# Kernel tuning notes

Measured on AMD Instinct MI355X. Metric: run time of the kernel, lower is better.

The kernel has to match this reference:

```python
import jax, jax.numpy as jnp
import numpy as np

B, S, HID = 2, 2048, 2048
NH, NKV, D = 32, 8, 128
EPS = 1e-06
ROPE_BASE = 1000000.0


def _rope_tables(seq_len, dim, base):
    inv_freq = 1.0 / (base ** (jnp.arange(0, dim, 2, dtype=jnp.float32) / dim))
    t = jnp.arange(seq_len, dtype=jnp.float32)
    freqs = jnp.einsum('i,j->ij', t, inv_freq)          # [S, D/2]
    emb = jnp.concatenate([freqs, freqs], axis=-1)      # [S, D]
    return emb[None, None].astype(jnp.float32)          # [1,1,S,D] (pre cos/sin)


def setup_inputs() -> dict:
    key = jax.random.key(0)
    ks = jax.random.split(key, 6)
    emb = _rope_tables(S, D, ROPE_BASE)
    return {
        'hidden_states': jax.random.normal(ks[0], (B, S, HID), jnp.float32),
        'cos': jnp.cos(emb),
        'sin': jnp.sin(emb),
        'wq': jax.random.normal(ks[1], (NH * D, HID), jnp.float32) * 0.02,
        'wk': jax.random.normal(ks[2], (NKV * D, HID), jnp.float32) * 0.02,
        'wv': jax.random.normal(ks[3], (NKV * D, HID), jnp.float32) * 0.02,
        'wo': jax.random.normal(ks[4], (HID, NH * D), jnp.float32) * 0.02,
        'q_norm_w': jnp.ones((D,), jnp.float32),
        'k_norm_w': jnp.ones((D,), jnp.float32),
    }


def _rmsnorm(x, w, eps=EPS):
    xf = x.astype(jnp.float32)
    var = jnp.mean(xf * xf, axis=-1, keepdims=True)
    return (w * (xf * jax.lax.rsqrt(var + eps))).astype(x.dtype)


def _rotate_half(x):
    x1, x2 = jnp.split(x, 2, axis=-1)
    return jnp.concatenate([-x2, x1], axis=-1)


def reference(hidden_states, cos, sin, wq, wk, wv, wo, q_norm_w, k_norm_w):
    b, s, _ = hidden_states.shape
    groups = NH // NKV
    # projections -> [b, heads, s, d]
    q = (hidden_states @ wq.T).reshape(b, s, NH, D).transpose(0, 2, 1, 3)
    k = (hidden_states @ wk.T).reshape(b, s, NKV, D).transpose(0, 2, 1, 3)
    v = (hidden_states @ wv.T).reshape(b, s, NKV, D).transpose(0, 2, 1, 3)
    # per-head RMSNorm then RoPE
    q = _rmsnorm(q, q_norm_w)
    k = _rmsnorm(k, k_norm_w)
    q = q * cos + _rotate_half(q) * sin
    k = k * cos + _rotate_half(k) * sin
    # GQA expansion (repeat_interleave on head dim)
    k = jnp.repeat(k, groups, axis=1)
    v = jnp.repeat(v, groups, axis=1)
    # attention scores with additive causal bias of -10000 (as in source)
    scores = jnp.einsum('bhqd,bhkd->bhqk', q, k) / jnp.sqrt(jnp.float32(D))
    mask = jnp.triu(jnp.ones((s, s), jnp.float32), k=1)
    scores = scores - mask * 10000.0
    attn = jax.nn.softmax(scores.astype(jnp.float32), axis=-1).astype(q.dtype)
    out = jnp.einsum('bhqk,bhkd->bhqd', attn, v)
    out = out.transpose(0, 2, 1, 3).reshape(b, s, NH * D)
    return out @ wo.T
```

## Files before the change

kernel.cpp:

```cpp
#include <hip/hip_runtime.h>

typedef unsigned short u16;
typedef __attribute__((ext_vector_type(8))) short bf16x8;
typedef __attribute__((ext_vector_type(4))) float f32x4;
typedef __attribute__((ext_vector_type(2))) unsigned int u32x2;
typedef __attribute__((ext_vector_type(4))) unsigned int u32x4;

#define GAS __attribute__((address_space(1)))
#define LAS __attribute__((address_space(3)))
#define MFMA __builtin_amdgcn_mfma_f32_16x16x32_bf16
#define BAR() __builtin_amdgcn_s_barrier()
#define WAITV(n) asm volatile("s_waitcnt vmcnt(" #n ")" ::: "memory")

__device__ __forceinline__ void gload16(const void* g, void* l) {
  __builtin_amdgcn_global_load_lds((GAS void*)g, (LAS void*)l, 16, 0, 0);
}
__device__ __forceinline__ u16 f2b(float x) {
  union { float f; unsigned u; } c; c.f = x;
  unsigned r = c.u + 0x7fffu + ((c.u >> 16) & 1u);
  return (u16)(r >> 16);
}
__device__ __forceinline__ float b2f(u16 h) {
  union { unsigned u; float f; } c; c.u = ((unsigned)h) << 16;
  return c.f;
}
__device__ __forceinline__ unsigned cvtpk(float lo, float hi) {
  unsigned r;
  asm("v_cvt_pk_bf16_f32 %0, %1, %2" : "=v"(r) : "v"(lo), "v"(hi));
  return r;
}

__global__ __launch_bounds__(256) void cvt_bf16(const float* __restrict__ src,
                                                u16* __restrict__ dst, int n8) {
  int i = blockIdx.x * 256 + threadIdx.x;
  if (i >= n8) return;
  const float4* s4 = (const float4*)src;
  float4 a = s4[(size_t)i * 2], b = s4[(size_t)i * 2 + 1];
  u32x4 v;
  v[0] = (unsigned)f2b(a.x) | ((unsigned)f2b(a.y) << 16);
  v[1] = (unsigned)f2b(a.z) | ((unsigned)f2b(a.w) << 16);
  v[2] = (unsigned)f2b(b.x) | ((unsigned)f2b(b.y) << 16);
  v[3] = (unsigned)f2b(b.z) | ((unsigned)f2b(b.w) << 16);
  *(u32x4*)(dst + (size_t)i * 8) = v;
}

template <int MODE>
__global__ __launch_bounds__(512, 2) void gemm256(
    const u16* __restrict__ A, const u16* __restrict__ B,
    u16* __restrict__ Dq, u16* __restrict__ Dk, u16* __restrict__ Dv,
    float* __restrict__ Dout, int K, int tilesN, int nwg) {
  __shared__ __attribute__((aligned(16))) u16 lds[2][2][2][128 * 64];
  const int tid = threadIdx.x;
  const int lane = tid & 63;
  const int w = tid >> 6;
  const int wr = w >> 2, wc = w & 3;
  const int r = lane & 15, g = lane >> 4;

  int wg = blockIdx.x;
  const int cpx = nwg >> 3;
  wg = (wg & 7) * cpx + (wg >> 3);
  const int bx = wg % tilesN, by = wg / tilesN;
  const size_t m0 = (size_t)by * 256, n0 = (size_t)bx * 256;
  const int NT = K >> 6;

  auto stage = [&](int dbuf, int op, int half, int c, int k0) {
    int slot = c * 512 + tid;
    int row = slot >> 3;
    int kg = (slot & 7) ^ (row & 7);
    const u16* src = (op == 0)
        ? A + (m0 + half * 128 + row) * (size_t)K + k0 + kg * 8
        : B + (n0 + half * 128 + row) * (size_t)K + k0 + kg * 8;
    gload16(src, (char*)&lds[dbuf][op][half][0] + c * 8192 + w * 1024);
  };
  auto ldA = [&](int cur, int mi, int kk) -> bf16x8 {
    int rowl = mi * 16 + r;
    return *(const bf16x8*)((const char*)&lds[cur][0][wr][0] + rowl * 128 +
                            (((kk << 2) + g) ^ (rowl & 7)) * 16);
  };
  auto ldB = [&](int cur, int ni, int kk) -> bf16x8 {
    int rowl = (wc & 1) * 64 + ni * 16 + r;
    return *(const bf16x8*)((const char*)&lds[cur][1][wc >> 1][0] + rowl * 128 +
                            (((kk << 2) + g) ^ (rowl & 7)) * 16);
  };

  f32x4 acc[8][4];
#pragma unroll
  for (int i = 0; i < 8; ++i)
#pragma unroll
    for (int j = 0; j < 4; ++j) acc[i][j] = (f32x4){0.f, 0.f, 0.f, 0.f};

  stage(0, 1, 0, 0, 0); stage(0, 1, 0, 1, 0);
  stage(0, 1, 1, 0, 0); stage(0, 1, 1, 1, 0);
  stage(0, 0, 0, 0, 0); stage(0, 0, 1, 0, 0);
  stage(0, 0, 0, 1, 0); stage(0, 0, 1, 1, 0);
  WAITV(2);
  BAR();

  bf16x8 bf_[4][2];

#define GPHASE(MI0, IS0, IS1, WAITCODE)                                    \
  {                                                                        \
    bf16x8 aA0 = ldA(cur, MI0, 0), aA1 = ldA(cur, MI0, 1);                 \
    bf16x8 aB0 = ldA(cur, MI0 + 1, 0), aB1 = ldA(cur, MI0 + 1, 1);         \
    IS0; IS1;                                                              \
    BAR();                                                                 \
    __builtin_amdgcn_s_setprio(1);                                         \
    _Pragma("unroll") for (int ni = 0; ni < 4; ++ni) {                     \
      acc[MI0][ni] = MFMA(aA0, bf_[ni][0], acc[MI0][ni], 0, 0, 0);         \
      acc[MI0][ni] = MFMA(aA1, bf_[ni][1], acc[MI0][ni], 0, 0, 0);         \
      acc[MI0 + 1][ni] = MFMA(aB0, bf_[ni][0], acc[MI0 + 1][ni], 0, 0, 0); \
      acc[MI0 + 1][ni] = MFMA(aB1, bf_[ni][1], acc[MI0 + 1][ni], 0, 0, 0); \
    }                                                                      \
    __builtin_amdgcn_s_setprio(0);                                         \
    WAITCODE;                                                              \
    BAR();                                                                 \
  }

  for (int t = 0; t < NT - 1; ++t) {
    const int cur = t & 1, nb = cur ^ 1;
    const int k1 = (t + 1) << 6;
#pragma unroll
    for (int ni = 0; ni < 4; ++ni) {
      bf_[ni][0] = ldB(cur, ni, 0);
      bf_[ni][1] = ldB(cur, ni, 1);
    }
    GPHASE(0, stage(nb, 1, 0, 0, k1), stage(nb, 1, 0, 1, k1), );
    GPHASE(2, stage(nb, 1, 1, 0, k1), stage(nb, 1, 1, 1, k1), WAITV(4));
    GPHASE(4, stage(nb, 0, 0, 0, k1), stage(nb, 0, 1, 0, k1), );
    GPHASE(6, stage(nb, 0, 0, 1, k1), stage(nb, 0, 1, 1, k1), WAITV(2));
  }
  {
    const int cur = (NT - 1) & 1;
#pragma unroll
    for (int ni = 0; ni < 4; ++ni) {
      bf_[ni][0] = ldB(cur, ni, 0);
      bf_[ni][1] = ldB(cur, ni, 1);
    }
    GPHASE(0, , , );
    GPHASE(2, , , WAITV(0));
    GPHASE(4, , , );
    GPHASE(6, , , );
  }
#undef GPHASE

#pragma unroll
  for (int mi = 0; mi < 8; ++mi)
#pragma unroll
    for (int ni = 0; ni < 4; ++ni)
#pragma unroll
      for (int j = 0; j < 4; ++j) {
        int m = (int)m0 + wr * 128 + mi * 16 + g * 4 + j;
        int n = (int)n0 + wc * 64 + ni * 16 + r;
        if (MODE == 0) {
          u16 hv = f2b(acc[mi][ni][j]);
          int b = m >> 11, s = m & 2047;
          if (n < 4096) {
            Dq[(((size_t)b * 32 + (n >> 7)) * 2048 + s) * 128 + (n & 127)] = hv;
          } else if (n < 5120) {
            int nn = n - 4096;
            Dk[(((size_t)b * 8 + (nn >> 7)) * 2048 + s) * 128 + (nn & 127)] = hv;
          } else {
            int nn = n - 5120;
            Dv[(((size_t)b * 8 + (nn >> 7)) * 2048 + s) * 128 + (nn & 127)] = hv;
          }
        } else {
          Dout[(size_t)m * (size_t)(tilesN * 256) + n] = acc[mi][ni][j];
        }
      }
}

__global__ __launch_bounds__(256) void transpose_v(const u16* __restrict__ V,
                                                   u16* __restrict__ VT) {
  __shared__ __attribute__((aligned(16))) u16 tile[64 * 72];
  const int tid = threadIdx.x;
  const int s0 = blockIdx.x * 64, d0 = blockIdx.y * 64, hz = blockIdx.z;
#pragma unroll
  for (int pp = 0; pp < 2; ++pp) {
    int row = pp * 32 + (tid >> 3), colg = tid & 7;
    u32x4 vv = *(const u32x4*)(V + ((size_t)hz * 2048 + s0 + row) * 128 + d0 + colg * 8);
    *(u32x4*)(&tile[row * 72 + colg * 8]) = vv;
  }
  __syncthreads();
#pragma unroll
  for (int pp = 0; pp < 2; ++pp) {
    int dr = pp * 32 + (tid >> 3), sg = tid & 7;
    u32x4 ov;
#pragma unroll
    for (int e2 = 0; e2 < 4; ++e2)
      ov[e2] = (unsigned)tile[(sg * 8 + 2 * e2) * 72 + dr] |
               ((unsigned)tile[(sg * 8 + 2 * e2 + 1) * 72 + dr] << 16);
    *(u32x4*)(VT + ((size_t)hz * 128 + d0 + dr) * 2048 + s0 + sg * 8) = ov;
  }
}

__global__ __launch_bounds__(256) void rms_rope(u16* __restrict__ X,
                                                const float* __restrict__ cosT,
                                                const float* __restrict__ sinT,
                                                const float* __restrict__ nw,
                                                int nrows, float oscale) {
  int idx = blockIdx.x * 256 + threadIdx.x;
  int row = idx >> 6;
  int lane = idx & 63;
  if (row >= nrows) return;
  int s = row & 2047;
  u16* rp = X + (size_t)row * 128;
  float x0 = b2f(rp[lane]);
  float x1 = b2f(rp[lane + 64]);
  float ss = x0 * x0 + x1 * x1;
#pragma unroll
  for (int m = 32; m >= 1; m >>= 1) ss += __shfl_xor(ss, m);
  float inv = rsqrtf(ss * (1.0f / 128.0f) + 1e-6f);
  x0 *= inv * nw[lane];
  x1 *= inv * nw[lane + 64];
  float c0 = cosT[s * 128 + lane], s0 = sinT[s * 128 + lane];
  float c1 = cosT[s * 128 + lane + 64], s1 = sinT[s * 128 + lane + 64];
  rp[lane] = f2b((x0 * c0 - x1 * s0) * oscale);
  rp[lane + 64] = f2b((x1 * c1 + x0 * s1) * oscale);
}

__global__ __launch_bounds__(256, 2) void attn_fwd(const u16* __restrict__ Q,
                                                   const u16* __restrict__ Kg,
                                                   const u16* __restrict__ Vg,
                                                   u16* __restrict__ AO) {
  __shared__ __attribute__((aligned(16))) u16 Ks[2][64 * 128];
  __shared__ __attribute__((aligned(16))) u16 Vt[2][128 * 64];
  __shared__ __attribute__((aligned(16))) u16 Plds[4][16 * 64];
  const int tid = threadIdx.x;
  const int lane = tid & 63;
  const int w = tid >> 6;
  const int r = lane & 15, g = lane >> 4;
  const int p = blockIdx.x, h = blockIdx.y, b = blockIdx.z;
  const int hkv = h >> 2;

  const u16* Kp = Kg + (((size_t)b * 8 + hkv) * 2048) * 128;
  const u16* Vp = Vg + (((size_t)b * 8 + hkv) * 128) * 2048;

  const short one_bf = (short)0x3F80;
  const bf16x8 vones = {one_bf, one_bf, one_bf, one_bf, one_bf, one_bf, one_bf, one_bf};

#pragma unroll 1
  for (int phase = 0; phase < 2; ++phase) {
    const int qt = phase == 0 ? (31 - p) : p;
    const u16* Qp = Q + (((size_t)b * 32 + h) * 2048 + qt * 64 + w * 16) * 128;

    bf16x8 qf[4];
#pragma unroll
    for (int kk = 0; kk < 4; ++kk)
      qf[kk] = *(const bf16x8*)(Qp + r * 128 + kk * 32 + g * 8);

    f32x4 off[8];
#pragma unroll
    for (int i = 0; i < 8; ++i) off[i] = (f32x4){0.f, 0.f, 0.f, 0.f};
    f32x4 lr4 = (f32x4){0.f, 0.f, 0.f, 0.f};
    float mrun = -1e30f;

    const u16* kst[4];
    const u16* vst[4];
#pragma unroll
    for (int c = 0; c < 4; ++c) {
      int t = c * 256 + tid;
      kst[c] = Kp + (size_t)(t >> 4) * 128 + (size_t)(((t & 15) ^ ((t >> 4) & 7)) * 8);
      int d = t >> 3;
      vst[c] = Vp + (size_t)d * 2048 + (size_t)(((t & 7) ^ ((d >> 1) & 7)) * 8);
    }
    auto stageKV = [&](int buf) {
#pragma unroll
      for (int c = 0; c < 4; ++c) {
        gload16(kst[c], (char*)&Ks[buf][0] + c * 4096 + w * 1024);
        kst[c] += 64 * 128;
      }
#pragma unroll
      for (int c = 0; c < 4; ++c) {
        gload16(vst[c], (char*)&Vt[buf][0] + c * 4096 + w * 1024);
        vst[c] += 64;
      }
    };

    const int qg = qt * 64 + w * 16 + r;
    const int nu = qt + 1;

    stageKV(0);
    WAITV(0);
    BAR();

    for (int kt = 0; kt < nu; ++kt) {
      const int cur = kt & 1;
      if (kt + 1 < nu) stageKV(cur ^ 1);

      const char* KsC = (const char*)&Ks[cur][0];
      const char* VtC = (const char*)&Vt[cur][0];

      f32x4 sc[4];
#pragma unroll
      for (int ni = 0; ni < 4; ++ni) {
        f32x4 a = (f32x4){0.f, 0.f, 0.f, 0.f};
        int ro = ni * 16 + r;
#pragma unroll
        for (int kk = 0; kk < 4; ++kk) {
          int slot = (ro * 16 + kk * 4 + g) ^ (ro & 7);
          bf16x8 kf = *(const bf16x8*)(KsC + slot * 16);
          a = MFMA(kf, qf[kk], a, 0, 0, 0);
        }
        sc[ni] = a;
      }

      float pm = -3e30f;
      if (kt == qt) {
#pragma unroll
        for (int ni = 0; ni < 4; ++ni)
#pragma unroll
          for (int j = 0; j < 4; ++j) {
            int kvg = kt * 64 + ni * 16 + g * 4 + j;
            float sv = sc[ni][j];
            sv = (kvg > qg) ? -1e30f : sv;
            sc[ni][j] = sv;
            pm = fmaxf(pm, sv);
          }
      } else {
#pragma unroll
        for (int ni = 0; ni < 4; ++ni)
#pragma unroll
          for (int j = 0; j < 4; ++j) pm = fmaxf(pm, sc[ni][j]);
      }
      pm = fmaxf(pm, __shfl_xor(pm, 16));
      pm = fmaxf(pm, __shfl_xor(pm, 32));

      if (__any(pm > mrun + 11.0f)) {
        float mn = fmaxf(mrun, pm);
        float sclq = exp2f(mrun - mn);
        mrun = mn;
        f32x4 sv4;
        sv4[0] = __shfl(sclq, g * 4 + 0);
        sv4[1] = __shfl(sclq, g * 4 + 1);
        sv4[2] = __shfl(sclq, g * 4 + 2);
        sv4[3] = __shfl(sclq, g * 4 + 3);
#pragma unroll
        for (int i = 0; i < 8; ++i) off[i] *= sv4;
        lr4 *= sv4;
      }

      unsigned pk[4][2];
#pragma unroll
      for (int ni = 0; ni < 4; ++ni) {
        float p0 = exp2f(sc[ni][0] - mrun);
        float p1 = exp2f(sc[ni][1] - mrun);
        float p2 = exp2f(sc[ni][2] - mrun);
        float p3 = exp2f(sc[ni][3] - mrun);
        pk[ni][0] = cvtpk(p0, p1);
        pk[ni][1] = cvtpk(p2, p3);
      }

      {
        char* pw = (char*)&Plds[w][0];
        int base = r * 128;
        int sw = (r & 7) << 4;
#pragma unroll
        for (int ni = 0; ni < 4; ++ni) {
          u32x2 pr; pr[0] = pk[ni][0]; pr[1] = pk[ni][1];
          *(u32x2*)(pw + ((base + ni * 32 + g * 8) ^ sw)) = pr;
        }
      }
      bf16x8 pa[2];
      {
        const char* pw = (const char*)&Plds[w][0];
        int sw = (r & 7) << 4;
#pragma unroll
        for (int kk = 0; kk < 2; ++kk)
          pa[kk] = *(const bf16x8*)(pw + ((r * 128 + kk * 64 + g * 16) ^ sw));
      }

      lr4 = MFMA(pa[0], vones, lr4, 0, 0, 0);
      lr4 = MFMA(pa[1], vones, lr4, 0, 0, 0);

#pragma unroll
      for (int dd = 0; dd < 8; ++dd) {
        int d = dd * 16 + r;
#pragma unroll
        for (int kk = 0; kk < 2; ++kk) {
          int ph = (kk * 4 + g) ^ ((r >> 1) & 7);
          bf16x8 vf = *(const bf16x8*)(VtC + (size_t)d * 128 + ph * 16);
          off[dd] = MFMA(pa[kk], vf, off[dd], 0, 0, 0);
        }
      }

      WAITV(0);
      BAR();
    }

    f32x4 il4;
#pragma unroll
    for (int j = 0; j < 4; ++j) il4[j] = 1.0f / lr4[j];
    const size_t ob = (size_t)b * 2048 + qt * 64 + w * 16 + g * 4;
#pragma unroll
    for (int dd = 0; dd < 8; ++dd) {
      AO[(ob + 0) * 4096 + h * 128 + dd * 16 + r] = f2b(off[dd][0] * il4[0]);
      AO[(ob + 1) * 4096 + h * 128 + dd * 16 + r] = f2b(off[dd][1] * il4[1]);
      AO[(ob + 2) * 4096 + h * 128 + dd * 16 + r] = f2b(off[dd][2] * il4[2]);
      AO[(ob + 3) * 4096 + h * 128 + dd * 16 + r] = f2b(off[dd][3] * il4[3]);
    }
  }
}

extern "C" void kernel_launch(void* const* d_in, const int* in_sizes, int n_in,
                              void* d_out, int out_size, void* d_ws, size_t ws_size,
                              hipStream_t stream) {
  (void)in_sizes; (void)n_in; (void)out_size; (void)ws_size;
  const float* hs = (const float*)d_in[0];
  const float* cosT = (const float*)d_in[1];
  const float* sinT = (const float*)d_in[2];
  const float* wq = (const float*)d_in[3];
  const float* wk = (const float*)d_in[4];
  const float* wv = (const float*)d_in[5];
  const float* wo = (const float*)d_in[6];
  const float* qnw = (const float*)d_in[7];
  const float* knw = (const float*)d_in[8];
  float* out = (float*)d_out;

  char* ws = (char*)d_ws;
  u16* hsb  = (u16*)(ws);
  u16* wqkv = (u16*)(ws + 16777216);
  u16* wob  = (u16*)(ws + 41943040);
  u16* Qb   = (u16*)(ws + 58720256);
  u16* Kb   = (u16*)(ws + 92274688);
  u16* VTb  = (u16*)(ws + 100663296);
  u16* AO   = (u16*)(ws + 109051904);
  u16* Vnrm = AO;

  cvt_bf16<<<4096, 256, 0, stream>>>(hs, hsb, 1048576);
  cvt_bf16<<<4096, 256, 0, stream>>>(wq, wqkv, 1048576);
  cvt_bf16<<<1024, 256, 0, stream>>>(wk, wqkv + (size_t)4096 * 2048, 262144);
  cvt_bf16<<<1024, 256, 0, stream>>>(wv, wqkv + (size_t)5120 * 2048, 262144);
  cvt_bf16<<<4096, 256, 0, stream>>>(wo, wob, 1048576);

  gemm256<0><<<384, 512, 0, stream>>>(hsb, wqkv, Qb, Kb, Vnrm, nullptr, 2048, 24, 384);

  transpose_v<<<dim3(32, 2, 16), 256, 0, stream>>>(Vnrm, VTb);

  rms_rope<<<32768, 256, 0, stream>>>(Qb, cosT, sinT, qnw, 131072,
                                      0.08838834764831845f * 1.4426950408889634f);
  rms_rope<<<8192, 256, 0, stream>>>(Kb, cosT, sinT, knw, 32768, 1.0f);

  attn_fwd<<<dim3(16, 32, 2), 256, 0, stream>>>(Qb, Kb, VTb, AO);

  gemm256<1><<<128, 512, 0, stream>>>(AO, wob, nullptr, nullptr, nullptr, out,
                                      4096, 8, 128);
}
```

Baseline: 397.2 us.

## Process 128-row query tiles per block with two 16-row fragments per wave

Each wave of the attention kernel now handles 32 query rows as two 16-row fragments, so every K and V fragment read from LDS feeds two MFMAs. The block's query tile grows from 64 to 128 rows and the grid halves to 8 blocks per head, with the causal pairing rebuilt around 16 tiles. This cuts K/V global and LDS traffic per query row. In exchange it roughly doubles accumulator registers (risking spills or lower occupancy), gives fewer blocks to spread over the CUs, and masks two whole KV tiles per diagonal.

Measured after the change: 386.2 us. 1.03x faster.

```diff
diff --git a/kernel.cpp b/kernel.cpp
--- a/kernel.cpp
+++ b/kernel.cpp
@@ -224,7 +224,7 @@
                                                    u16* __restrict__ AO) {
   __shared__ __attribute__((aligned(16))) u16 Ks[2][64 * 128];
   __shared__ __attribute__((aligned(16))) u16 Vt[2][128 * 64];
-  __shared__ __attribute__((aligned(16))) u16 Plds[4][16 * 64];
+  __shared__ __attribute__((aligned(16))) u16 Plds[4][32 * 64];
   const int tid = threadIdx.x;
   const int lane = tid & 63;
   const int w = tid >> 6;
@@ -240,19 +240,25 @@
 
 #pragma unroll 1
   for (int phase = 0; phase < 2; ++phase) {
-    const int qt = phase == 0 ? (31 - p) : p;
-    const u16* Qp = Q + (((size_t)b * 32 + h) * 2048 + qt * 64 + w * 16) * 128;
-
-    bf16x8 qf[4];
-#pragma unroll
-    for (int kk = 0; kk < 4; ++kk)
-      qf[kk] = *(const bf16x8*)(Qp + r * 128 + kk * 32 + g * 8);
-
-    f32x4 off[8];
-#pragma unroll
-    for (int i = 0; i < 8; ++i) off[i] = (f32x4){0.f, 0.f, 0.f, 0.f};
-    f32x4 lr4 = (f32x4){0.f, 0.f, 0.f, 0.f};
-    float mrun = -1e30f;
+    const int qt = phase == 0 ? (15 - p) : p;
+    const u16* Qp = Q + (((size_t)b * 32 + h) * 2048 + qt * 128 + w * 32) * 128;
+
+    bf16x8 qf[2][4];
+#pragma unroll
+    for (int f = 0; f < 2; ++f)
+#pragma unroll
+      for (int kk = 0; kk < 4; ++kk)
+        qf[f][kk] = *(const bf16x8*)(Qp + (f * 16 + r) * 128 + kk * 32 + g * 8);
+
+    f32x4 off[2][8];
+#pragma unroll
+    for (int f = 0; f < 2; ++f)
+#pragma unroll
+      for (int i = 0; i < 8; ++i) off[f][i] = (f32x4){0.f, 0.f, 0.f, 0.f};
+    f32x4 lr4[2] = {(f32x4){0.f, 0.f, 0.f, 0.f}, (f32x4){0.f, 0.f, 0.f, 0.f}};
+    float mrun[2] = {-1e30f, -1e30f};
+    const int qg0 = qt * 128 + w * 32 + r;
+    const int qg1 = qg0 + 16;
 
     const u16* kst[4];
     const u16* vst[4];
@@ -276,8 +282,7 @@
       }
     };
 
-    const int qg = qt * 64 + w * 16 + r;
-    const int nu = qt + 1;
+    const int nu = 2 * qt + 2;
 
     stageKV(0);
     WAITV(0);
@@ -290,87 +295,106 @@
       const char* KsC = (const char*)&Ks[cur][0];
       const char* VtC = (const char*)&Vt[cur][0];
 
-      f32x4 sc[4];
+      f32x4 sc0[4], sc1[4];
 #pragma unroll
       for (int ni = 0; ni < 4; ++ni) {
-        f32x4 a = (f32x4){0.f, 0.f, 0.f, 0.f};
+        f32x4 a0 = (f32x4){0.f, 0.f, 0.f, 0.f};
+        f32x4 a1 = (f32x4){0.f, 0.f, 0.f, 0.f};
         int ro = ni * 16 + r;
 #pragma unroll
         for (int kk = 0; kk < 4; ++kk) {
           int slot = (ro * 16 + kk * 4 + g) ^ (ro & 7);
           bf16x8 kf = *(const bf16x8*)(KsC + slot * 16);
-          a = MFMA(kf, qf[kk], a, 0, 0, 0);
+          a0 = MFMA(kf, qf[0][kk], a0, 0, 0, 0);
+          a1 = MFMA(kf, qf[1][kk], a1, 0, 0, 0);
         }
-        sc[ni] = a;
-      }
-
-      float pm = -3e30f;
-      if (kt == qt) {
+        sc0[ni] = a0;
+        sc1[ni] = a1;
+      }
+
+      float pm0 = -3e30f, pm1 = -3e30f;
+      if (kt >= 2 * qt) {
 #pragma unroll
         for (int ni = 0; ni < 4; ++ni)
 #pragma unroll
           for (int j = 0; j < 4; ++j) {
             int kvg = kt * 64 + ni * 16 + g * 4 + j;
-            float sv = sc[ni][j];
-            sv = (kvg > qg) ? -1e30f : sv;
-            sc[ni][j] = sv;
-            pm = fmaxf(pm, sv);
+            float s0 = sc0[ni][j], s1 = sc1[ni][j];
+            s0 = (kvg > qg0) ? -1e30f : s0;
+            s1 = (kvg > qg1) ? -1e30f : s1;
+            sc0[ni][j] = s0; sc1[ni][j] = s1;
+            pm0 = fmaxf(pm0, s0); pm1 = fmaxf(pm1, s1);
           }
       } else {
 #pragma unroll
         for (int ni = 0; ni < 4; ++ni)
 #pragma unroll
-          for (int j = 0; j < 4; ++j) pm = fmaxf(pm, sc[ni][j]);
-      }
-      pm = fmaxf(pm, __shfl_xor(pm, 16));
-      pm = fmaxf(pm, __shfl_xor(pm, 32));
-
-      if (__any(pm > mrun + 11.0f)) {
-        float mn = fmaxf(mrun, pm);
-        float sclq = exp2f(mrun - mn);
-        mrun = mn;
+          for (int j = 0; j < 4; ++j) {
+            pm0 = fmaxf(pm0, sc0[ni][j]);
+            pm1 = fmaxf(pm1, sc1[ni][j]);
+          }
+      }
+      pm0 = fmaxf(pm0, __shfl_xor(pm0, 16));
+      pm0 = fmaxf(pm0, __shfl_xor(pm0, 32));
+      pm1 = fmaxf(pm1, __shfl_xor(pm1, 16));
+      pm1 = fmaxf(pm1, __shfl_xor(pm1, 32));
+
+      if (__any(pm0 > mrun[0] + 11.0f)) {
+        float mn = fmaxf(mrun[0], pm0);
+        float sclq = exp2f(mrun[0] - mn);
+        mrun[0] = mn;
         f32x4 sv4;
         sv4[0] = __shfl(sclq, g * 4 + 0);
         sv4[1] = __shfl(sclq, g * 4 + 1);
         sv4[2] = __shfl(sclq, g * 4 + 2);
         sv4[3] = __shfl(sclq, g * 4 + 3);
 #pragma unroll
-        for (int i = 0; i < 8; ++i) off[i] *= sv4;
-        lr4 *= sv4;
-      }
-
-      unsigned pk[4][2];
-#pragma unroll
-      for (int ni = 0; ni < 4; ++ni) {
-        float p0 = exp2f(sc[ni][0] - mrun);
-        float p1 = exp2f(sc[ni][1] - mrun);
-        float p2 = exp2f(sc[ni][2] - mrun);
-        float p3 = exp2f(sc[ni][3] - mrun);
-        pk[ni][0] = cvtpk(p0, p1);
-        pk[ni][1] = cvtpk(p2, p3);
+        for (int i = 0; i < 8; ++i) off[0][i] *= sv4;
+        lr4[0] *= sv4;
+      }
+      if (__any(pm1 > mrun[1] + 11.0f)) {
+        float mn = fmaxf(mrun[1], pm1);
+        float sclq = exp2f(mrun[1] - mn);
+        mrun[1] = mn;
+        f32x4 sv4;
+        sv4[0] = __shfl(sclq, g * 4 + 0);
+        sv4[1] = __shfl(sclq, g * 4 + 1);
+        sv4[2] = __shfl(sclq, g * 4 + 2);
+        sv4[3] = __shfl(sclq, g * 4 + 3);
+#pragma unroll
+        for (int i = 0; i < 8; ++i) off[1][i] *= sv4;
+        lr4[1] *= sv4;
       }
 
       {
         char* pw = (char*)&Plds[w][0];
-        int base = r * 128;
         int sw = (r & 7) << 4;
 #pragma unroll
         for (int ni = 0; ni < 4; ++ni) {
-          u32x2 pr; pr[0] = pk[ni][0]; pr[1] = pk[ni][1];
-          *(u32x2*)(pw + ((base + ni * 32 + g * 8) ^ sw)) = pr;
+          u32x2 pr0, pr1;
+          pr0[0] = cvtpk(exp2f(sc0[ni][0] - mrun[0]), exp2f(sc0[ni][1] - mrun[0]));
+          pr0[1] = cvtpk(exp2f(sc0[ni][2] - mrun[0]), exp2f(sc0[ni][3] - mrun[0]));
+          pr1[0] = cvtpk(exp2f(sc1[ni][0] - mrun[1]), exp2f(sc1[ni][1] - mrun[1]));
+          pr1[1] = cvtpk(exp2f(sc1[ni][2] - mrun[1]), exp2f(sc1[ni][3] - mrun[1]));
+          *(u32x2*)(pw + ((r * 128 + ni * 32 + g * 8) ^ sw)) = pr0;
+          *(u32x2*)(pw + (((16 + r) * 128 + ni * 32 + g * 8) ^ sw)) = pr1;
         }
       }
-      bf16x8 pa[2];
+      bf16x8 pa[2][2];
       {
         const char* pw = (const char*)&Plds[w][0];
         int sw = (r & 7) << 4;
 #pragma unroll
-        for (int kk = 0; kk < 2; ++kk)
-          pa[kk] = *(const bf16x8*)(pw + ((r * 128 + kk * 64 + g * 16) ^ sw));
-      }
-
-      lr4 = MFMA(pa[0], vones, lr4, 0, 0, 0);
-      lr4 = MFMA(pa[1], vones, lr4, 0, 0, 0);
+        for (int kk = 0; kk < 2; ++kk) {
+          pa[0][kk] = *(const bf16x8*)(pw + ((r * 128 + kk * 64 + g * 16) ^ sw));
+          pa[1][kk] = *(const bf16x8*)(pw + (((16 + r) * 128 + kk * 64 + g * 16) ^ sw));
+        }
+      }
+
+      lr4[0] = MFMA(pa[0][0], vones, lr4[0], 0, 0, 0);
+      lr4[0] = MFMA(pa[0][1], vones, lr4[0], 0, 0, 0);
+      lr4[1] = MFMA(pa[1][0], vones, lr4[1], 0, 0, 0);
+      lr4[1] = MFMA(pa[1][1], vones, lr4[1], 0, 0, 0);
 
 #pragma unroll
       for (int dd = 0; dd < 8; ++dd) {
@@ -379,7 +403,8 @@
         for (int kk = 0; kk < 2; ++kk) {
           int ph = (kk * 4 + g) ^ ((r >> 1) & 7);
           bf16x8 vf = *(const bf16x8*)(VtC + (size_t)d * 128 + ph * 16);
-          off[dd] = MFMA(pa[kk], vf, off[dd], 0, 0, 0);
+          off[0][dd] = MFMA(pa[0][kk], vf, off[0][dd], 0, 0, 0);
+          off[1][dd] = MFMA(pa[1][kk], vf, off[1][dd], 0, 0, 0);
         }
       }
 
@@ -387,16 +412,19 @@
       BAR();
     }
 
-    f32x4 il4;
-#pragma unroll
-    for (int j = 0; j < 4; ++j) il4[j] = 1.0f / lr4[j];
-    const size_t ob = (size_t)b * 2048 + qt * 64 + w * 16 + g * 4;
-#pragma unroll
-    for (int dd = 0; dd < 8; ++dd) {
-      AO[(ob + 0) * 4096 + h * 128 + dd * 16 + r] = f2b(off[dd][0] * il4[0]);
-      AO[(ob + 1) * 4096 + h * 128 + dd * 16 + r] = f2b(off[dd][1] * il4[1]);
-      AO[(ob + 2) * 4096 + h * 128 + dd * 16 + r] = f2b(off[dd][2] * il4[2]);
-      AO[(ob + 3) * 4096 + h * 128 + dd * 16 + r] = f2b(off[dd][3] * il4[3]);
+#pragma unroll
+    for (int f = 0; f < 2; ++f) {
+      f32x4 il4;
+#pragma unroll
+      for (int j = 0; j < 4; ++j) il4[j] = 1.0f / lr4[f][j];
+      const size_t ob = (size_t)b * 2048 + qt * 128 + w * 32 + f * 16 + g * 4;
+#pragma unroll
+      for (int dd = 0; dd < 8; ++dd) {
+        AO[(ob + 0) * 4096 + h * 128 + dd * 16 + r] = f2b(off[f][dd][0] * il4[0]);
+        AO[(ob + 1) * 4096 + h * 128 + dd * 16 + r] = f2b(off[f][dd][1] * il4[1]);
+        AO[(ob + 2) * 4096 + h * 128 + dd * 16 + r] = f2b(off[f][dd][2] * il4[2]);
+        AO[(ob + 3) * 4096 + h * 128 + dd * 16 + r] = f2b(off[f][dd][3] * il4[3]);
+      }
     }
   }
 }
@@ -440,7 +468,7 @@
                                       0.08838834764831845f * 1.4426950408889634f);
   rms_rope<<<8192, 256, 0, stream>>>(Kb, cosT, sinT, knw, 32768, 1.0f);
 
-  attn_fwd<<<dim3(16, 32, 2), 256, 0, stream>>>(Qb, Kb, VTb, AO);
+  attn_fwd<<<dim3(8, 32, 2), 256, 0, stream>>>(Qb, Kb, VTb, AO);
 
   gemm256<1><<<128, 512, 0, stream>>>(AO, wob, nullptr, nullptr, nullptr, out,
                                       4096, 8, 128);
```
